# Kernel optimization log

Hardware: AMD Instinct MI355X
Metric: run time of the kernel (lower is better)

The kernel has to match this reference:

```python
import jax, jax.numpy as jnp
import numpy as np

DIM = 1024
HIDDEN = 4096
NUM_EXPERTS = 8
TOP_K = 2


def setup_inputs() -> dict:
    key = jax.random.key(0)
    ks = jax.random.split(key, 7)
    x = jax.random.normal(ks[0], (4, 2048, DIM), dtype=jnp.float32)
    # router Linear(dim, num_experts)
    Wr = jax.random.normal(ks[1], (DIM, NUM_EXPERTS), dtype=jnp.float32) / np.sqrt(DIM)
    br = jnp.zeros((NUM_EXPERTS,), dtype=jnp.float32)
    # stacked expert weights: Linear(dim, hidden) -> GELU -> Linear(hidden, dim)
    W1 = jax.random.normal(ks[2], (NUM_EXPERTS, DIM, HIDDEN), dtype=jnp.float32) / np.sqrt(DIM)
    b1 = jnp.zeros((NUM_EXPERTS, HIDDEN), dtype=jnp.float32)
    W2 = jax.random.normal(ks[3], (NUM_EXPERTS, HIDDEN, DIM), dtype=jnp.float32) / np.sqrt(HIDDEN)
    b2 = jnp.zeros((NUM_EXPERTS, DIM), dtype=jnp.float32)
    return {"x": x, "Wr": Wr, "br": br, "W1": W1, "b1": b1, "W2": W2, "b2": b2}


def reference(x, Wr, br, W1, b1, W2, b2):
    # router: g_x = W_e x ; p = softmax(g_x)
    logits = jnp.einsum('bsd,de->bse', x, Wr) + br            # [B,S,E]
    probs = jax.nn.softmax(logits, axis=-1)
    topk_probs, topk_idx = jax.lax.top_k(probs, TOP_K)        # [B,S,K]
    # dense compute-all-experts (faithful to torch.stack over experts)
    h = jnp.einsum('bsd,edh->bseh', x, W1) + b1               # [B,S,E,H]
    h = jax.nn.gelu(h, approximate=False)                      # torch nn.GELU default = exact erf
    expert_out = jnp.einsum('bseh,ehd->bsed', h, W2) + b2     # [B,S,E,D]
    # gather top-k expert outputs and mix
    selected = jnp.take_along_axis(expert_out, topk_idx[..., None], axis=2)  # [B,S,K,D]
    mixed = jnp.sum(topk_probs[..., None] * selected, axis=2)                # [B,S,D]
    return mixed, logits, probs, topk_idx, topk_probs
```

## Files before the change

### kernel.cpp

```cpp
#include <hip/hip_runtime.h>
#include <hip/hip_bf16.h>
#include <math.h>
#include <stdint.h>

#define DIMD 1024
#define HIDDEN 4096
#define NE 8
#define TOPK_ 2
#define T_TOKENS 8192
#define NROWS (T_TOKENS * TOPK_)
#define BK 64
#define BM1 128
#define BN1 256
#define BM2 128
#define BN2 128
#define MAXTILES (NROWS / 128 + NE)
#define TGS 8
#define SPLITK 2
#define NRB (T_TOKENS / 8)

typedef __bf16 bf16_t;
typedef __bf16 bf16x8 __attribute__((ext_vector_type(8)));
typedef float f32x4 __attribute__((ext_vector_type(4)));

__device__ __forceinline__ void glds16(const void* g, void* l) {
    __builtin_amdgcn_global_load_lds(
        (const __attribute__((address_space(1))) unsigned int*)g,
        (__attribute__((address_space(3))) unsigned int*)l, 16, 0, 0);
}

__device__ __forceinline__ bf16x8 ldfrag(const char* lds_, int row, int kelem) {
    int byte = row * 128 + ((kelem * 2) ^ ((row & 7) << 4));
    return *reinterpret_cast<const bf16x8*>(lds_ + byte);
}

__device__ __forceinline__ int xcd_contig(int bid, int nwg) {
    int xcd = bid & 7;
    int lid = bid >> 3;
    int q = nwg >> 3, r = nwg & 7;
    int base = (xcd < r) ? xcd * (q + 1) : r * (q + 1) + (xcd - r) * q;
    return base + lid;
}

__global__ __launch_bounds__(512) void prologue_kernel(
    const float* __restrict__ x, const float* __restrict__ Wr, const float* __restrict__ br,
    const float* __restrict__ W1, const float* __restrict__ W2,
    float* __restrict__ logits, float* __restrict__ probs,
    float* __restrict__ tidx, float* __restrict__ tprob,
    int* __restrict__ cnt, bf16_t* __restrict__ Xb,
    bf16_t* __restrict__ W1T, bf16_t* __restrict__ W2T)
{
    __shared__ float tile[128][132];
    int bid0 = blockIdx.x;
    if (bid0 < NRB) {
        int wave = threadIdx.x >> 6;
        int lane = threadIdx.x & 63;
        int t = bid0 * 8 + wave;
        const float* xr = x + (size_t)t * DIMD;
        double acc[NE];
#pragma unroll
        for (int e = 0; e < NE; ++e) acc[e] = 0.0;
        for (int i = 0; i < DIMD / 64; ++i) {
            int d = i * 64 + lane;
            double xv = (double)xr[d];
            float4 w0 = *reinterpret_cast<const float4*>(Wr + d * NE);
            float4 w1 = *reinterpret_cast<const float4*>(Wr + d * NE + 4);
            acc[0] += xv * (double)w0.x; acc[1] += xv * (double)w0.y;
            acc[2] += xv * (double)w0.z; acc[3] += xv * (double)w0.w;
            acc[4] += xv * (double)w1.x; acc[5] += xv * (double)w1.y;
            acc[6] += xv * (double)w1.z; acc[7] += xv * (double)w1.w;
        }
#pragma unroll
        for (int s = 32; s >= 1; s >>= 1) {
#pragma unroll
            for (int e = 0; e < NE; ++e) acc[e] += __shfl_xor(acc[e], s, 64);
        }
        if (lane == 0) {
            double lg[NE], mx = -1e300;
#pragma unroll
            for (int e = 0; e < NE; ++e) { lg[e] = acc[e] + (double)br[e]; mx = fmax(mx, lg[e]); }
            int i0 = 0; double l0 = -1e300;
#pragma unroll
            for (int e = 0; e < NE; ++e) { if (lg[e] > l0) { l0 = lg[e]; i0 = e; } }
            int i1 = -1; double l1 = -1e300;
#pragma unroll
            for (int e = 0; e < NE; ++e) { if (e == i0) continue; if (lg[e] > l1) { l1 = lg[e]; i1 = e; } }
            float pe[NE], s = 0.f;
#pragma unroll
            for (int e = 0; e < NE; ++e) { pe[e] = __expf((float)(lg[e] - mx)); s += pe[e]; }
            float inv = 1.f / s;
#pragma unroll
            for (int e = 0; e < NE; ++e) {
                pe[e] *= inv;
                logits[t * NE + e] = (float)lg[e];
                probs[t * NE + e] = pe[e];
            }
            tidx[t * 2 + 0] = (float)i0; tidx[t * 2 + 1] = (float)i1;
            tprob[t * 2 + 0] = pe[i0];   tprob[t * 2 + 1] = pe[i1];
            atomicAdd(&cnt[i0], 1); atomicAdd(&cnt[i1], 1);
        }
#pragma unroll
        for (int j = 0; j < 2; ++j) {
            int i = (j * 64 + lane) * 8;
            float4 a = *reinterpret_cast<const float4*>(xr + i);
            float4 b = *reinterpret_cast<const float4*>(xr + i + 4);
            bf16x8 o;
            o[0] = (bf16_t)a.x; o[1] = (bf16_t)a.y; o[2] = (bf16_t)a.z; o[3] = (bf16_t)a.w;
            o[4] = (bf16_t)b.x; o[5] = (bf16_t)b.y; o[6] = (bf16_t)b.z; o[7] = (bf16_t)b.w;
            *reinterpret_cast<bf16x8*>(Xb + (size_t)t * DIMD + i) = o;
        }
        return;
    }
    int bid = bid0 - NRB;
    const float* in; bf16_t* out; int K, N, kt, nt, e;
    if (bid < 2048) {
        in = W1; out = W1T; K = DIMD; N = HIDDEN;
        e = bid >> 8; int rem = bid & 255;
        kt = rem >> 5; nt = rem & 31;
    } else {
        bid -= 2048;
        in = W2; out = W2T; K = HIDDEN; N = DIMD;
        e = bid >> 8; int rem = bid & 255;
        kt = rem >> 3; nt = rem & 7;
    }
    int k0 = kt * 128;
    int n0 = nt * 128;
    const float* ip = in + (size_t)e * K * N + (size_t)k0 * N + n0;
    bf16_t* op = out + (size_t)e * N * K + (size_t)n0 * K + k0;
    int t = threadIdx.x;
    int r = t >> 2;
    int q = t & 3;
    const float* rp = ip + (size_t)r * N + q * 32;
#pragma unroll
    for (int i = 0; i < 8; ++i) {
        float4 v = *reinterpret_cast<const float4*>(rp + i * 4);
        *reinterpret_cast<float4*>(&tile[r][q * 32 + i * 4]) = v;
    }
    __syncthreads();
    int nn = t >> 2;
    bf16_t* wp = op + (size_t)nn * K + q * 32;
#pragma unroll
    for (int i = 0; i < 4; ++i) {
        bf16x8 o;
#pragma unroll
        for (int j = 0; j < 8; ++j) o[j] = (bf16_t)tile[q * 32 + i * 8 + j][nn];
        *reinterpret_cast<bf16x8*>(wp + i * 8) = o;
    }
}

__global__ __launch_bounds__(256) void prefix_kernel(
    const int* __restrict__ cnt, int* __restrict__ offsets,
    int* __restrict__ tileE, int* __restrict__ tileRow, int* __restrict__ numTiles)
{
    __shared__ int soff[NE + 1], scnt[NE];
    int t = threadIdx.x;
    if (t == 0) {
        int off = 0;
        for (int e = 0; e < NE; ++e) { scnt[e] = cnt[e]; soff[e] = off; off += scnt[e]; }
        soff[NE] = off;
        int nt = 0;
        for (int e = 0; e < NE; ++e) nt += (scnt[e] + 127) / 128;
        *numTiles = nt;
    }
    __syncthreads();
    if (t <= NE) offsets[t] = soff[t];
    if (t < MAXTILES) {
        int acc = 0;
#pragma unroll
        for (int e = 0; e < NE; ++e) {
            int ntE = (scnt[e] + 127) / 128;
            if (t < acc + ntE) { tileE[t] = e; tileRow[t] = soff[e] + (t - acc) * 128; return; }
            acc += ntE;
        }
    }
}

__global__ __launch_bounds__(256) void scatter_kernel(
    const float* __restrict__ tidx, const float* __restrict__ tprob,
    const int* __restrict__ offsets, int* __restrict__ gcursor,
    int* __restrict__ rowToken, float* __restrict__ rowProb)
{
    __shared__ int lcnt[NE], lbase[NE];
    int t = blockIdx.x * 256 + threadIdx.x;
    if (threadIdx.x < NE) lcnt[threadIdx.x] = 0;
    __syncthreads();
    int e0 = (int)tidx[t * 2 + 0], e1 = (int)tidx[t * 2 + 1];
    float p0 = tprob[t * 2 + 0],   p1 = tprob[t * 2 + 1];
    int r0l = atomicAdd(&lcnt[e0], 1);
    int r1l = atomicAdd(&lcnt[e1], 1);
    __syncthreads();
    if (threadIdx.x < NE) lbase[threadIdx.x] = atomicAdd(&gcursor[threadIdx.x], lcnt[threadIdx.x]);
    __syncthreads();
    int r0 = offsets[e0] + lbase[e0] + r0l;
    int r1 = offsets[e1] + lbase[e1] + r1l;
    rowToken[r0] = t; rowProb[r0] = p0;
    rowToken[r1] = t; rowProb[r1] = p1;
}

__global__ __launch_bounds__(512) void ffn1_kernel(
    const bf16_t* __restrict__ Xb, const bf16_t* __restrict__ W1T, const float* __restrict__ b1,
    const int* __restrict__ tileE, const int* __restrict__ tileRow, const int* __restrict__ numTiles,
    const int* __restrict__ offsets, const int* __restrict__ rowToken,
    bf16_t* __restrict__ h)
{
    const int NB = HIDDEN / BN1;
    int logical = xcd_contig(blockIdx.x, gridDim.x);
    int tg  = logical / (NB * TGS);
    int rem = logical % (NB * TGS);
    int nb  = rem / TGS;
    int ti  = rem % TGS;
    int tile = tg * TGS + ti;
    if (tile >= *numTiles) return;
    int e = tileE[tile];
    int row0 = tileRow[tile];
    int rend = offsets[e + 1];
    int n0 = nb * BN1;

    __shared__ __align__(16) char lds[49152];

    int tid = threadIdx.x;
    int lane = tid & 63;
    int wid = tid >> 6;
    int wr = (wid >> 2) * 64;
    int wc = (wid & 3) * 64;
    int rr = lane & 15;
    int k4 = (lane >> 4) * 8;

    int srow = tid >> 3;
    int xc = (((tid & 7) ^ (srow & 7)) << 4);
    const char *pa0, *pa1, *pb0, *pb1, *pb2, *pb3;
    {
        int g0 = row0 + srow;      if (g0 > NROWS - 1) g0 = NROWS - 1;
        int g1 = row0 + 64 + srow; if (g1 > NROWS - 1) g1 = NROWS - 1;
        pa0 = (const char*)(Xb + (size_t)rowToken[g0] * DIMD) + xc;
        pa1 = (const char*)(Xb + (size_t)rowToken[g1] * DIMD) + xc;
        pb0 = (const char*)(W1T + ((size_t)e * HIDDEN + n0 + srow) * DIMD) + xc;
        pb1 = (const char*)(W1T + ((size_t)e * HIDDEN + n0 + 64 + srow) * DIMD) + xc;
        pb2 = (const char*)(W1T + ((size_t)e * HIDDEN + n0 + 128 + srow) * DIMD) + xc;
        pb3 = (const char*)(W1T + ((size_t)e * HIDDEN + n0 + 192 + srow) * DIMD) + xc;
    }

    f32x4 acc[4][4];
#pragma unroll
    for (int i = 0; i < 4; ++i)
#pragma unroll
        for (int j = 0; j < 4; ++j) acc[i][j] = f32x4{0.f, 0.f, 0.f, 0.f};

    for (int t_ = 0; t_ < DIMD / BK; ++t_) {
        int kb = t_ * 128;
        glds16(pa0 + kb, lds + wid * 1024);
        glds16(pa1 + kb, lds + 8192 + wid * 1024);
        glds16(pb0 + kb, lds + 16384 + wid * 1024);
        glds16(pb1 + kb, lds + 24576 + wid * 1024);
        glds16(pb2 + kb, lds + 32768 + wid * 1024);
        glds16(pb3 + kb, lds + 40960 + wid * 1024);
        __syncthreads();
#pragma unroll
        for (int ks = 0; ks < 2; ++ks) {
            int kk = ks * 32 + k4;
            bf16x8 b_[4], a_[4];
#pragma unroll
            for (int n = 0; n < 4; ++n) b_[n] = ldfrag(lds + 16384, wc + n * 16 + rr, kk);
#pragma unroll
            for (int m = 0; m < 4; ++m) a_[m] = ldfrag(lds, wr + m * 16 + rr, kk);
#pragma unroll
            for (int m = 0; m < 4; ++m)
#pragma unroll
                for (int n = 0; n < 4; ++n)
                    acc[m][n] = __builtin_amdgcn_mfma_f32_16x16x32_bf16(a_[m], b_[n], acc[m][n], 0, 0, 0);
        }
        __syncthreads();
    }

    int crow = (lane >> 4) * 4;
    int ccol = lane & 15;
#pragma unroll
    for (int m = 0; m < 4; ++m) {
#pragma unroll
        for (int n = 0; n < 4; ++n) {
            int col = wc + n * 16 + ccol;
            float bias = b1[e * HIDDEN + n0 + col];
#pragma unroll
            for (int r = 0; r < 4; ++r) {
                int row = row0 + wr + m * 16 + crow + r;
                if (row < rend) {
                    float v = acc[m][n][r] + bias;
                    float g = 0.5f * v * (1.0f + erff(v * 0.70710678118654752f));
                    h[(size_t)row * HIDDEN + n0 + col] = (bf16_t)g;
                }
            }
        }
    }
}

__global__ __launch_bounds__(256) void ffn2_kernel(
    const bf16_t* __restrict__ h, const bf16_t* __restrict__ W2T, const float* __restrict__ b2,
    const int* __restrict__ tileE, const int* __restrict__ tileRow, const int* __restrict__ numTiles,
    const int* __restrict__ offsets, const int* __restrict__ rowToken, const float* __restrict__ rowProb,
    float* __restrict__ mixed)
{
    const int NB = DIMD / BN2;
    int logical = xcd_contig(blockIdx.x, gridDim.x);
    int z = logical / (MAXTILES * NB);
    int rem = logical % (MAXTILES * NB);
    int tile = rem / NB;
    int nb = rem % NB;
    if (tile >= *numTiles) return;
    int e = tileE[tile];
    int row0 = tileRow[tile];
    int rend = offsets[e + 1];
    int n0 = nb * BN2;
    const int khalf = HIDDEN / SPLITK;
    int khb = z * khalf * 2;

    __shared__ __align__(16) char lds[32768];

    int tid = threadIdx.x;
    int lane = tid & 63;
    int wid = tid >> 6;
    int wr = (wid >> 1) * 64;
    int wc = (wid & 1) * 64;
    int rr = lane & 15;
    int k4 = (lane >> 4) * 8;

    int srow = tid >> 3;
    int xc = (((tid & 7) ^ (srow & 7)) << 4);
    const char *pa0, *pa1, *pa2, *pa3, *pb0, *pb1, *pb2, *pb3;
    {
        int g0 = row0 + srow;      if (g0 > NROWS - 1) g0 = NROWS - 1;
        int g1 = row0 + 32 + srow; if (g1 > NROWS - 1) g1 = NROWS - 1;
        int g2 = row0 + 64 + srow; if (g2 > NROWS - 1) g2 = NROWS - 1;
        int g3 = row0 + 96 + srow; if (g3 > NROWS - 1) g3 = NROWS - 1;
        pa0 = (const char*)(h + (size_t)g0 * HIDDEN) + khb + xc;
        pa1 = (const char*)(h + (size_t)g1 * HIDDEN) + khb + xc;
        pa2 = (const char*)(h + (size_t)g2 * HIDDEN) + khb + xc;
        pa3 = (const char*)(h + (size_t)g3 * HIDDEN) + khb + xc;
        pb0 = (const char*)(W2T + ((size_t)e * DIMD + n0 + srow) * HIDDEN) + khb + xc;
        pb1 = (const char*)(W2T + ((size_t)e * DIMD + n0 + 32 + srow) * HIDDEN) + khb + xc;
        pb2 = (const char*)(W2T + ((size_t)e * DIMD + n0 + 64 + srow) * HIDDEN) + khb + xc;
        pb3 = (const char*)(W2T + ((size_t)e * DIMD + n0 + 96 + srow) * HIDDEN) + khb + xc;
    }

    f32x4 acc[4][4];
#pragma unroll
    for (int i = 0; i < 4; ++i)
#pragma unroll
        for (int j = 0; j < 4; ++j) acc[i][j] = f32x4{0.f, 0.f, 0.f, 0.f};

    for (int t_ = 0; t_ < khalf / BK; ++t_) {
        int kb = t_ * 128;
        char* dA = lds + wid * 1024;
        char* dB = lds + 16384 + wid * 1024;
        glds16(pa0 + kb, dA);          glds16(pb0 + kb, dB);
        glds16(pa1 + kb, dA + 4096);   glds16(pb1 + kb, dB + 4096);
        glds16(pa2 + kb, dA + 8192);   glds16(pb2 + kb, dB + 8192);
        glds16(pa3 + kb, dA + 12288);  glds16(pb3 + kb, dB + 12288);
        __syncthreads();
#pragma unroll
        for (int ks = 0; ks < 2; ++ks) {
            int kk = ks * 32 + k4;
            bf16x8 a_[4], b_[4];
#pragma unroll
            for (int m = 0; m < 4; ++m) a_[m] = ldfrag(lds, wr + m * 16 + rr, kk);
#pragma unroll
            for (int n = 0; n < 4; ++n) b_[n] = ldfrag(lds + 16384, wc + n * 16 + rr, kk);
#pragma unroll
            for (int m = 0; m < 4; ++m)
#pragma unroll
                for (int n = 0; n < 4; ++n)
                    acc[m][n] = __builtin_amdgcn_mfma_f32_16x16x32_bf16(a_[m], b_[n], acc[m][n], 0, 0, 0);
        }
        __syncthreads();
    }

    int crow = (lane >> 4) * 4;
    int ccol = lane & 15;
    int dobias = (z == 0);
#pragma unroll
    for (int m = 0; m < 4; ++m) {
#pragma unroll
        for (int n = 0; n < 4; ++n) {
            int col = wc + n * 16 + ccol;
            int dcol = n0 + col;
            float bias = dobias ? b2[e * DIMD + dcol] : 0.f;
#pragma unroll
            for (int r = 0; r < 4; ++r) {
                int row = row0 + wr + m * 16 + crow + r;
                if (row < rend) {
                    float v = acc[m][n][r] + bias;
                    float p = rowProb[row];
                    int tok = rowToken[row];
                    atomicAdd(&mixed[(size_t)tok * DIMD + dcol], p * v);
                }
            }
        }
    }
}

extern "C" void kernel_launch(void* const* d_in, const int* in_sizes, int n_in,
                              void* d_out, int out_size, void* d_ws, size_t ws_size,
                              hipStream_t stream)
{
    const float* x  = (const float*)d_in[0];
    const float* Wr = (const float*)d_in[1];
    const float* br = (const float*)d_in[2];
    const float* W1 = (const float*)d_in[3];
    const float* b1 = (const float*)d_in[4];
    const float* W2 = (const float*)d_in[5];
    const float* b2 = (const float*)d_in[6];

    float* out = (float*)d_out;
    float* mixed  = out;
    float* logits = out + (size_t)T_TOKENS * DIMD;
    float* probs  = logits + T_TOKENS * NE;
    float* tidx   = probs + T_TOKENS * NE;
    float* tprob  = tidx + T_TOKENS * TOPK_;

    char* p = (char*)d_ws;
    auto alloc = [&](size_t bytes) { char* r = p; p += (bytes + 255) & ~255ull; return r; };
    int*    small    = (int*)alloc(2 * NE * 4);
    int*    cnt      = small;
    int*    gcursor  = small + NE;
    int*    offsets  = (int*)alloc((NE + 1) * 4);
    int*    numTiles = (int*)alloc(4);
    int*    tileE    = (int*)alloc(MAXTILES * 4);
    int*    tileRow  = (int*)alloc(MAXTILES * 4);
    int*    rowToken = (int*)alloc(NROWS * 4);
    float*  rowProb  = (float*)alloc(NROWS * 4);
    bf16_t* W1T      = (bf16_t*)alloc((size_t)NE * HIDDEN * DIMD * 2);
    bf16_t* W2T      = (bf16_t*)alloc((size_t)NE * DIMD * HIDDEN * 2);
    bf16_t* Xb       = (bf16_t*)alloc((size_t)T_TOKENS * DIMD * 2);
    bf16_t* hbuf     = (bf16_t*)alloc((size_t)NROWS * HIDDEN * 2);

    hipMemsetAsync(small, 0, 2 * NE * 4, stream);
    hipMemsetAsync(mixed, 0, (size_t)T_TOKENS * DIMD * 4, stream);

    prologue_kernel<<<NRB + 4096, 512, 0, stream>>>(
        x, Wr, br, W1, W2, logits, probs, tidx, tprob, cnt, Xb, W1T, W2T);
    prefix_kernel<<<1, 256, 0, stream>>>(cnt, offsets, tileE, tileRow, numTiles);
    scatter_kernel<<<T_TOKENS / 256, 256, 0, stream>>>(tidx, tprob, offsets, gcursor, rowToken, rowProb);

    ffn1_kernel<<<MAXTILES * (HIDDEN / BN1), 512, 0, stream>>>(
        Xb, W1T, b1, tileE, tileRow, numTiles, offsets, rowToken, hbuf);
    ffn2_kernel<<<MAXTILES * (DIMD / BN2) * SPLITK, 256, 0, stream>>>(
        hbuf, W2T, b2, tileE, tileRow, numTiles, offsets, rowToken, rowProb, mixed);
}
```

Measured before the change: 779.4 us.

## Replace split-K atomic scatter in FFN2 with per-row partials and a gather reduce

The second expert GEMM drops its split-K of 2 and no longer does float atomicAdds into the mixed output. Each routed row now writes its biased result to a per-row fp32 partial buffer. A new reduce kernel gathers each token's two rows, weights them by the top-k probabilities and writes the output directly, so the output memset is no longer needed. This removes atomic contention and makes the result deterministic, at the cost of an extra 64 MB fp32 buffer round-trip, one more launch, and half as many FFN2 workgroups.

```diff
diff --git a/kernel.cpp b/kernel.cpp
--- a/kernel.cpp
+++ b/kernel.cpp
@@ -16,7 +16,6 @@
 #define BN2 128
 #define MAXTILES (NROWS / 128 + NE)
 #define TGS 8
-#define SPLITK 2
 #define NRB (T_TOKENS / 8)
 
 typedef __bf16 bf16_t;
@@ -178,14 +177,13 @@
 __global__ __launch_bounds__(256) void scatter_kernel(
     const float* __restrict__ tidx, const float* __restrict__ tprob,
     const int* __restrict__ offsets, int* __restrict__ gcursor,
-    int* __restrict__ rowToken, float* __restrict__ rowProb)
+    int* __restrict__ rowToken, int* __restrict__ tokRow)
 {
     __shared__ int lcnt[NE], lbase[NE];
     int t = blockIdx.x * 256 + threadIdx.x;
     if (threadIdx.x < NE) lcnt[threadIdx.x] = 0;
     __syncthreads();
     int e0 = (int)tidx[t * 2 + 0], e1 = (int)tidx[t * 2 + 1];
-    float p0 = tprob[t * 2 + 0],   p1 = tprob[t * 2 + 1];
     int r0l = atomicAdd(&lcnt[e0], 1);
     int r1l = atomicAdd(&lcnt[e1], 1);
     __syncthreads();
@@ -193,8 +191,8 @@
     __syncthreads();
     int r0 = offsets[e0] + lbase[e0] + r0l;
     int r1 = offsets[e1] + lbase[e1] + r1l;
-    rowToken[r0] = t; rowProb[r0] = p0;
-    rowToken[r1] = t; rowProb[r1] = p1;
+    rowToken[r0] = t; rowToken[r1] = t;
+    tokRow[t * 2 + 0] = r0; tokRow[t * 2 + 1] = r1;
 }
 
 __global__ __launch_bounds__(512) void ffn1_kernel(
@@ -296,22 +294,17 @@
 __global__ __launch_bounds__(256) void ffn2_kernel(
     const bf16_t* __restrict__ h, const bf16_t* __restrict__ W2T, const float* __restrict__ b2,
     const int* __restrict__ tileE, const int* __restrict__ tileRow, const int* __restrict__ numTiles,
-    const int* __restrict__ offsets, const int* __restrict__ rowToken, const float* __restrict__ rowProb,
-    float* __restrict__ mixed)
+    const int* __restrict__ offsets, float* __restrict__ part)
 {
     const int NB = DIMD / BN2;
     int logical = xcd_contig(blockIdx.x, gridDim.x);
-    int z = logical / (MAXTILES * NB);
-    int rem = logical % (MAXTILES * NB);
-    int tile = rem / NB;
-    int nb = rem % NB;
+    int tile = logical / NB;
+    int nb = logical % NB;
     if (tile >= *numTiles) return;
     int e = tileE[tile];
     int row0 = tileRow[tile];
     int rend = offsets[e + 1];
     int n0 = nb * BN2;
-    const int khalf = HIDDEN / SPLITK;
-    int khb = z * khalf * 2;
 
     __shared__ __align__(16) char lds[32768];
 
@@ -331,14 +324,14 @@
         int g1 = row0 + 32 + srow; if (g1 > NROWS - 1) g1 = NROWS - 1;
         int g2 = row0 + 64 + srow; if (g2 > NROWS - 1) g2 = NROWS - 1;
         int g3 = row0 + 96 + srow; if (g3 > NROWS - 1) g3 = NROWS - 1;
-        pa0 = (const char*)(h + (size_t)g0 * HIDDEN) + khb + xc;
-        pa1 = (const char*)(h + (size_t)g1 * HIDDEN) + khb + xc;
-        pa2 = (const char*)(h + (size_t)g2 * HIDDEN) + khb + xc;
-        pa3 = (const char*)(h + (size_t)g3 * HIDDEN) + khb + xc;
-        pb0 = (const char*)(W2T + ((size_t)e * DIMD + n0 + srow) * HIDDEN) + khb + xc;
-        pb1 = (const char*)(W2T + ((size_t)e * DIMD + n0 + 32 + srow) * HIDDEN) + khb + xc;
-        pb2 = (const char*)(W2T + ((size_t)e * DIMD + n0 + 64 + srow) * HIDDEN) + khb + xc;
-        pb3 = (const char*)(W2T + ((size_t)e * DIMD + n0 + 96 + srow) * HIDDEN) + khb + xc;
+        pa0 = (const char*)(h + (size_t)g0 * HIDDEN) + xc;
+        pa1 = (const char*)(h + (size_t)g1 * HIDDEN) + xc;
+        pa2 = (const char*)(h + (size_t)g2 * HIDDEN) + xc;
+        pa3 = (const char*)(h + (size_t)g3 * HIDDEN) + xc;
+        pb0 = (const char*)(W2T + ((size_t)e * DIMD + n0 + srow) * HIDDEN) + xc;
+        pb1 = (const char*)(W2T + ((size_t)e * DIMD + n0 + 32 + srow) * HIDDEN) + xc;
+        pb2 = (const char*)(W2T + ((size_t)e * DIMD + n0 + 64 + srow) * HIDDEN) + xc;
+        pb3 = (const char*)(W2T + ((size_t)e * DIMD + n0 + 96 + srow) * HIDDEN) + xc;
     }
 
     f32x4 acc[4][4];
@@ -347,7 +340,7 @@
 #pragma unroll
         for (int j = 0; j < 4; ++j) acc[i][j] = f32x4{0.f, 0.f, 0.f, 0.f};
 
-    for (int t_ = 0; t_ < khalf / BK; ++t_) {
+    for (int t_ = 0; t_ < HIDDEN / BK; ++t_) {
         int kb = t_ * 128;
         char* dA = lds + wid * 1024;
         char* dB = lds + 16384 + wid * 1024;
@@ -375,26 +368,41 @@
 
     int crow = (lane >> 4) * 4;
     int ccol = lane & 15;
-    int dobias = (z == 0);
 #pragma unroll
     for (int m = 0; m < 4; ++m) {
 #pragma unroll
         for (int n = 0; n < 4; ++n) {
             int col = wc + n * 16 + ccol;
             int dcol = n0 + col;
-            float bias = dobias ? b2[e * DIMD + dcol] : 0.f;
+            float bias = b2[e * DIMD + dcol];
 #pragma unroll
             for (int r = 0; r < 4; ++r) {
                 int row = row0 + wr + m * 16 + crow + r;
                 if (row < rend) {
-                    float v = acc[m][n][r] + bias;
-                    float p = rowProb[row];
-                    int tok = rowToken[row];
-                    atomicAdd(&mixed[(size_t)tok * DIMD + dcol], p * v);
+                    part[(size_t)row * DIMD + dcol] = acc[m][n][r] + bias;
                 }
             }
         }
     }
+}
+
+__global__ __launch_bounds__(256) void reduce_kernel(
+    const float* __restrict__ part, const float* __restrict__ tprob,
+    const int* __restrict__ tokRow, float* __restrict__ mixed)
+{
+    int idx = blockIdx.x * 256 + threadIdx.x;
+    int tok = idx >> 8;
+    int q = (idx & 255) * 4;
+    int r0 = tokRow[tok * 2 + 0], r1 = tokRow[tok * 2 + 1];
+    float p0 = tprob[tok * 2 + 0], p1 = tprob[tok * 2 + 1];
+    float4 a = *reinterpret_cast<const float4*>(part + (size_t)r0 * DIMD + q);
+    float4 b = *reinterpret_cast<const float4*>(part + (size_t)r1 * DIMD + q);
+    float4 o;
+    o.x = p0 * a.x + p1 * b.x;
+    o.y = p0 * a.y + p1 * b.y;
+    o.z = p0 * a.z + p1 * b.z;
+    o.w = p0 * a.w + p1 * b.w;
+    *reinterpret_cast<float4*>(mixed + (size_t)tok * DIMD + q) = o;
 }
 
 extern "C" void kernel_launch(void* const* d_in, const int* in_sizes, int n_in,
@@ -426,22 +434,23 @@
     int*    tileE    = (int*)alloc(MAXTILES * 4);
     int*    tileRow  = (int*)alloc(MAXTILES * 4);
     int*    rowToken = (int*)alloc(NROWS * 4);
-    float*  rowProb  = (float*)alloc(NROWS * 4);
+    int*    tokRow   = (int*)alloc(NROWS * 4);
     bf16_t* W1T      = (bf16_t*)alloc((size_t)NE * HIDDEN * DIMD * 2);
     bf16_t* W2T      = (bf16_t*)alloc((size_t)NE * DIMD * HIDDEN * 2);
     bf16_t* Xb       = (bf16_t*)alloc((size_t)T_TOKENS * DIMD * 2);
     bf16_t* hbuf     = (bf16_t*)alloc((size_t)NROWS * HIDDEN * 2);
+    float*  part     = (float*)alloc((size_t)NROWS * DIMD * 4);
 
     hipMemsetAsync(small, 0, 2 * NE * 4, stream);
-    hipMemsetAsync(mixed, 0, (size_t)T_TOKENS * DIMD * 4, stream);
 
     prologue_kernel<<<NRB + 4096, 512, 0, stream>>>(
         x, Wr, br, W1, W2, logits, probs, tidx, tprob, cnt, Xb, W1T, W2T);
     prefix_kernel<<<1, 256, 0, stream>>>(cnt, offsets, tileE, tileRow, numTiles);
-    scatter_kernel<<<T_TOKENS / 256, 256, 0, stream>>>(tidx, tprob, offsets, gcursor, rowToken, rowProb);
+    scatter_kernel<<<T_TOKENS / 256, 256, 0, stream>>>(tidx, tprob, offsets, gcursor, rowToken, tokRow);
 
     ffn1_kernel<<<MAXTILES * (HIDDEN / BN1), 512, 0, stream>>>(
         Xb, W1T, b1, tileE, tileRow, numTiles, offsets, rowToken, hbuf);
-    ffn2_kernel<<<MAXTILES * (DIMD / BN2) * SPLITK, 256, 0, stream>>>(
-        hbuf, W2T, b2, tileE, tileRow, numTiles, offsets, rowToken, rowProb, mixed);
-}
+    ffn2_kernel<<<MAXTILES * (DIMD / BN2), 256, 0, stream>>>(
+        hbuf, W2T, b2, tileE, tileRow, numTiles, offsets, part);
+    reduce_kernel<<<T_TOKENS * DIMD / 4 / 256, 256, 0, stream>>>(part, tprob, tokRow, mixed);
+}
```

After: 717.1 us, median of 2. -8.0%, faster.
